# Kernel tuning notes

Hardware: AMD Instinct MI355X
Metric: run time of the kernel (lower is better)

## Reference

```python
import jax, jax.numpy as jnp
import numpy as np

NUM_EXPERTS = 8
M_TOTAL = 16384      # total routed tokens, sorted by expert
IN_FEATURES = 2048
OUT_FEATURES = 2048


def setup_inputs() -> dict:
    key = jax.random.key(0)
    k1, k2 = jax.random.split(key)
    x = jax.random.normal(k1, (M_TOTAL, IN_FEATURES), dtype=jnp.float32)
    # moe_fused_kaiming_uniform_: uniform(-sqrt(3*5/in), +sqrt(3*5/in))
    bound = float(np.sqrt(3.0 * 5.0 / IN_FEATURES))
    weight = jax.random.uniform(
        k2, (NUM_EXPERTS, OUT_FEATURES, IN_FEATURES),
        dtype=jnp.float32, minval=-bound, maxval=bound)
    # variable-size expert groups that sum exactly to M_TOTAL
    rng = np.random.default_rng(0)
    cuts = np.sort(rng.choice(np.arange(1, M_TOTAL), NUM_EXPERTS - 1, replace=False))
    m_sizes = np.diff(np.concatenate([[0], cuts, [M_TOTAL]])).astype(np.int32)
    return {"input": x, "weight": weight, "m_sizes": jnp.asarray(m_sizes)}


def reference(input, weight, m_sizes):
    """Grouped GEMM: rows of `input` are sorted by expert; the e-th contiguous
    block of m_sizes[e] rows is multiplied by weight[e].T ([out, in] -> x @ W_e^T)."""
    num_experts, out_features, _ = weight.shape
    m = input.shape[0]
    # per-token expert id from group sizes (jit-safe: fixed total length)
    expert_ids = jnp.repeat(jnp.arange(num_experts, dtype=jnp.int32), m_sizes,
                            total_repeat_length=m)  # [M]
    out = jnp.zeros((m, out_features), dtype=input.dtype)
    for e in range(num_experts):  # small fixed expert count
        mask = (expert_ids == e)[:, None]
        out = out + jnp.where(mask, input @ weight[e].T, jnp.zeros((), input.dtype))
    return out
```

## Files before the change

### kernel.cpp

```cpp
#include <hip/hip_runtime.h>
#include <hip/hip_bf16.h>

#define M_TOTAL 16384
#define KDIM 2048
#define NDIM 2048
#define NEXP 8
#define BM 256
#define BN 256
#define BK 32
#define MAX_ROW_TILES 71
#define NWG (MAX_ROW_TILES * 8)

typedef __attribute__((ext_vector_type(8))) __bf16 bf16x8;
typedef __attribute__((ext_vector_type(4))) float f32x4;

__device__ inline int minI(int a, int b) { return a < b ? a : b; }

__device__ inline bf16x8 cvt8(float4 a, float4 b) {
  bf16x8 r;
  r[0] = (__bf16)a.x; r[1] = (__bf16)a.y; r[2] = (__bf16)a.z; r[3] = (__bf16)a.w;
  r[4] = (__bf16)b.x; r[5] = (__bf16)b.y; r[6] = (__bf16)b.z; r[7] = (__bf16)b.w;
  return r;
}

__device__ inline void gload16(const void* g, void* l) {
  __builtin_amdgcn_global_load_lds(
      (const __attribute__((address_space(1))) void*)g,
      (__attribute__((address_space(3))) void*)l, 16, 0, 0);
}

__global__ __launch_bounds__(256) void cvt_both(
    const float* __restrict__ x, const float* __restrict__ w,
    bf16x8* __restrict__ xb, bf16x8* __restrict__ wb) {
  const int NX = (M_TOTAL * KDIM) / 8;
  const int NW = (NEXP * NDIM * KDIM) / 8;
  const int stride = gridDim.x * blockDim.x;
  for (int i = blockIdx.x * blockDim.x + threadIdx.x; i < NX + NW; i += stride) {
    const float4* src = (i < NX) ? ((const float4*)x + (size_t)i * 2)
                                 : ((const float4*)w + (size_t)(i - NX) * 2);
    float4 a = src[0], b = src[1];
    bf16x8 c = cvt8(a, b);
    if (i < NX) xb[i] = c; else wb[i - NX] = c;
  }
}

__global__ __launch_bounds__(512, 2) void moe_gemm_fr(
    const __hip_bfloat16* __restrict__ xb, const __hip_bfloat16* __restrict__ wb,
    const int* __restrict__ ms, float* __restrict__ out) {
  __shared__ __align__(16) char lds[131072];

  const int orig = blockIdx.x;
  const int wg = (orig & 7) * MAX_ROW_TILES + (orig >> 3);
  const int bt = wg >> 3;
  const int ntile = wg & 7;

  int sizes[NEXP];
#pragma unroll
  for (int i = 0; i < NEXP; ++i) sizes[i] = ms[i];
  int e = 0, row0 = 0, rows = 0, acc_t = 0, start = 0;
  bool found = false;
#pragma unroll
  for (int i = 0; i < NEXP; ++i) {
    int nt = (sizes[i] + BM - 1) >> 8;
    if (!found && bt < acc_t + nt) {
      found = true; e = i;
      int tt = bt - acc_t;
      row0 = start + tt * BM;
      rows = minI(sizes[i] - tt * BM, BM);
    }
    acc_t += nt; start += sizes[i];
  }
  if (!found) return;

  const int tid = threadIdx.x;
  const int lane = tid & 63;
  const int wave = tid >> 6;
  const int wr = wave >> 2, wc = wave & 3;
  const int col0 = ntile * BN;

  const int rwh = wave * 16 + (lane >> 2);
  const int colel = (((lane & 3) ^ ((lane >> 3) & 3)) << 3);
  const __hip_bfloat16* aS0 = xb + (size_t)minI(row0 + rwh, M_TOTAL - 1) * KDIM + colel;
  const __hip_bfloat16* aS1 = xb + (size_t)minI(row0 + 128 + rwh, M_TOTAL - 1) * KDIM + colel;
  const __hip_bfloat16* wbase = wb + (size_t)e * NDIM * KDIM;
  const __hip_bfloat16* bS0 = wbase + (size_t)(col0 + rwh) * KDIM + colel;
  const __hip_bfloat16* bS1 = wbase + (size_t)(col0 + 128 + rwh) * KDIM + colel;

  const int fr = lane & 15, fc = lane >> 4;
  const int laneOff = fr * 64 + ((fc ^ ((fr >> 1) & 3)) << 4);
  const int aOff = wr * 8192 + laneOff;
  const int bOff = 16384 + (wc >> 1) * 8192 + (wc & 1) * 4096 + laneOff;

  f32x4 acc[8][4];
  const f32x4 zero = {0.f, 0.f, 0.f, 0.f};
#pragma unroll
  for (int i = 0; i < 8; ++i)
#pragma unroll
    for (int j = 0; j < 4; ++j) acc[i][j] = zero;

#define ST4(BI, T) { char* b_ = lds + (BI) * 32768 + wave * 1024; \
    gload16(aS0 + (size_t)(T) * BK, b_); \
    gload16(aS1 + (size_t)(T) * BK, b_ + 8192); \
    gload16(bS0 + (size_t)(T) * BK, b_ + 16384); \
    gload16(bS1 + (size_t)(T) * BK, b_ + 24576); }
#define VM4 "vmcnt(4)"
#define VM0 "vmcnt(0)"

#define TILE(BI, T, DOST, VM) { \
    asm volatile("s_waitcnt " VM); \
    __builtin_amdgcn_s_barrier(); \
    if (DOST) ST4(((BI) + 2) & 3, (T) + 2); \
    const char* bb_ = lds + (BI) * 32768; \
    bf16x8 af[8], bv[4]; \
    bv[0] = *(const bf16x8*)(bb_ + bOff); \
    _Pragma("unroll") for (int mt = 0; mt < 8; ++mt) \
      af[mt] = *(const bf16x8*)(bb_ + aOff + mt * 1024); \
    _Pragma("unroll") for (int nt = 1; nt < 4; ++nt) \
      bv[nt] = *(const bf16x8*)(bb_ + bOff + nt * 1024); \
    __builtin_amdgcn_s_setprio(1); \
    _Pragma("unroll") for (int nt = 0; nt < 4; ++nt) \
      _Pragma("unroll") for (int mt = 0; mt < 8; ++mt) \
        acc[mt][nt] = __builtin_amdgcn_mfma_f32_16x16x32_bf16( \
            af[mt], bv[nt], acc[mt][nt], 0, 0, 0); \
    __builtin_amdgcn_s_setprio(0); \
  }

  ST4(0, 0)
  ST4(1, 1)

  for (int i = 0; i < 15; ++i) {
    const int t = 4 * i;
    TILE(0, t,     true, VM4)
    TILE(1, t + 1, true, VM4)
    TILE(2, t + 2, true, VM4)
    TILE(3, t + 3, true, VM4)
  }
  TILE(0, 60, true,  VM4)
  TILE(1, 61, true,  VM4)
  TILE(2, 62, false, VM4)
  TILE(3, 63, false, VM0)

#undef TILE
#undef VM0
#undef VM4
#undef ST4

  const int er = (lane >> 4) * 4;
#pragma unroll
  for (int mt = 0; mt < 8; ++mt) {
#pragma unroll
    for (int j = 0; j < 4; ++j) {
      int r = wr * 128 + mt * 16 + er + j;
      if (r < rows) {
        float* op = out + (size_t)(row0 + r) * NDIM + col0 + wc * 64 + (lane & 15);
#pragma unroll
        for (int nt = 0; nt < 4; ++nt) op[nt * 16] = acc[mt][nt][j];
      }
    }
  }
}

__global__ __launch_bounds__(256) void moe_gemm_f32(
    const float* __restrict__ x, const float* __restrict__ w,
    const int* __restrict__ ms, float* __restrict__ out) {
  __shared__ __align__(16) char As[128 * 64 * 2];
  __shared__ __align__(16) char Bs[128 * 64 * 2];
  int sizes[NEXP];
#pragma unroll
  for (int i = 0; i < NEXP; ++i) sizes[i] = ms[i];
  const int bt = blockIdx.y;
  int e = 0, row0 = 0, rows = 0, acc_t = 0, start = 0;
  bool found = false;
#pragma unroll
  for (int i = 0; i < NEXP; ++i) {
    int nt = (sizes[i] + 127) >> 7;
    if (!found && bt < acc_t + nt) {
      found = true; e = i;
      int tt = bt - acc_t;
      row0 = start + tt * 128;
      rows = minI(sizes[i] - tt * 128, 128);
    }
    acc_t += nt; start += sizes[i];
  }
  if (!found) return;
  const int tid = threadIdx.x;
  const int lane = tid & 63;
  const int wave = tid >> 6;
  const int wm = wave >> 1, wn = wave & 1;
  const int col0 = blockIdx.x * 128;
  const float* wbase = w + (size_t)e * (size_t)NDIM * KDIM;
  const int sr = tid >> 1;
  const int sh = tid & 1;
  const float* aptr = x + (size_t)(row0 + sr) * KDIM + sh * 32;
  const float* bptr = wbase + (size_t)(col0 + sr) * KDIM + sh * 32;
  const bool aval = (sr < rows);
  f32x4 acc[4][4];
  const f32x4 zero = {0.f, 0.f, 0.f, 0.f};
#pragma unroll
  for (int i = 0; i < 4; ++i)
#pragma unroll
    for (int j = 0; j < 4; ++j) acc[i][j] = zero;
  for (int kb = 0; kb < KDIM / 64; ++kb) {
    {
      float4 v[8];
      if (aval) {
        const float4* p = (const float4*)(aptr + kb * 64);
#pragma unroll
        for (int j = 0; j < 8; ++j) v[j] = p[j];
      } else {
#pragma unroll
        for (int j = 0; j < 8; ++j) v[j] = make_float4(0.f, 0.f, 0.f, 0.f);
      }
#pragma unroll
      for (int j = 0; j < 4; ++j) {
        bf16x8 c = cvt8(v[2 * j], v[2 * j + 1]);
        int chunk = (sh * 4 + j) ^ (sr & 7);
        *(bf16x8*)(As + sr * 128 + chunk * 16) = c;
      }
    }
    {
      const float4* p = (const float4*)(bptr + kb * 64);
      float4 u[8];
#pragma unroll
      for (int j = 0; j < 8; ++j) u[j] = p[j];
#pragma unroll
      for (int j = 0; j < 4; ++j) {
        bf16x8 c = cvt8(u[2 * j], u[2 * j + 1]);
        int chunk = (sh * 4 + j) ^ (sr & 7);
        *(bf16x8*)(Bs + sr * 128 + chunk * 16) = c;
      }
    }
    __syncthreads();
#pragma unroll
    for (int ks = 0; ks < 2; ++ks) {
      bf16x8 afr[4], bfv[4];
#pragma unroll
      for (int mt = 0; mt < 4; ++mt) {
        int r = wm * 64 + mt * 16 + (lane & 15);
        int chunk = (ks * 4 + (lane >> 4)) ^ (r & 7);
        afr[mt] = *(const bf16x8*)(As + r * 128 + chunk * 16);
      }
#pragma unroll
      for (int nt = 0; nt < 4; ++nt) {
        int r = wn * 64 + nt * 16 + (lane & 15);
        int chunk = (ks * 4 + (lane >> 4)) ^ (r & 7);
        bfv[nt] = *(const bf16x8*)(Bs + r * 128 + chunk * 16);
      }
#pragma unroll
      for (int mt = 0; mt < 4; ++mt)
#pragma unroll
        for (int nt = 0; nt < 4; ++nt)
          acc[mt][nt] = __builtin_amdgcn_mfma_f32_16x16x32_bf16(
              afr[mt], bfv[nt], acc[mt][nt], 0, 0, 0);
    }
    __syncthreads();
  }
#pragma unroll
  for (int mt = 0; mt < 4; ++mt) {
#pragma unroll
    for (int j = 0; j < 4; ++j) {
      int r = wm * 64 + mt * 16 + (lane >> 4) * 4 + j;
      if (r < rows) {
        float* op = out + (size_t)(row0 + r) * NDIM + col0 + wn * 64 + (lane & 15);
#pragma unroll
        for (int nt = 0; nt < 4; ++nt) op[nt * 16] = acc[mt][nt][j];
      }
    }
  }
}

extern "C" void kernel_launch(void* const* d_in, const int* in_sizes, int n_in,
                              void* d_out, int out_size, void* d_ws, size_t ws_size,
                              hipStream_t stream) {
  const float* x = (const float*)d_in[0];
  const float* w = (const float*)d_in[1];
  const int* ms = (const int*)d_in[2];
  float* out = (float*)d_out;
  const size_t nx = (size_t)M_TOTAL * KDIM;
  const size_t nw = (size_t)NEXP * NDIM * KDIM;
  const size_t need = (nx + nw) * sizeof(__hip_bfloat16);
  if (ws_size >= need) {
    __hip_bfloat16* xb = (__hip_bfloat16*)d_ws;
    __hip_bfloat16* wb = xb + nx;
    cvt_both<<<2048, 256, 0, stream>>>(x, w, (bf16x8*)xb, (bf16x8*)wb);
    moe_gemm_fr<<<dim3(NWG), dim3(512), 0, stream>>>(xb, wb, ms, out);
  } else {
    moe_gemm_f32<<<dim3(16, 135), dim3(256), 0, stream>>>(x, w, ms, out);
  }
}
```

Baseline: 249.0 us.

## Double-buffer A fragments in registers and deepen global prefetch to three tiles

The GEMM main loop now loads the A-operand fragments for the next K-tile from LDS into a second register set while the MFMAs for the current tile run, alternating between two register buffers. Global-to-LDS prefetch distance is raised from two tiles ahead to three, with a prologue that stages three tiles and preloads the first A fragments. The aim is to hide LDS read latency behind MFMA work and give global loads more slack. The cost is eight more bf16x8 registers per thread under a 2-waves-per-SIMD launch bound, which could cause spills, and tighter reuse of the four LDS buffers.

```diff
diff --git a/kernel.cpp b/kernel.cpp
--- a/kernel.cpp
+++ b/kernel.cpp
@@ -44,7 +44,7 @@
   }
 }
 
-__global__ __launch_bounds__(512, 2) void moe_gemm_fr(
+__global__ __launch_bounds__(512, 2) void moe_gemm_rdb(
     const __hip_bfloat16* __restrict__ xb, const __hip_bfloat16* __restrict__ wb,
     const int* __restrict__ ms, float* __restrict__ out) {
   __shared__ __align__(16) char lds[131072];
@@ -98,6 +98,8 @@
 #pragma unroll
     for (int j = 0; j < 4; ++j) acc[i][j] = zero;
 
+  bf16x8 afX[8], afY[8];
+
 #define ST4(BI, T) { char* b_ = lds + (BI) * 32768 + wave * 1024; \
     gload16(aS0 + (size_t)(T) * BK, b_); \
     gload16(aS1 + (size_t)(T) * BK, b_ + 8192); \
@@ -106,39 +108,45 @@
 #define VM4 "vmcnt(4)"
 #define VM0 "vmcnt(0)"
 
-#define TILE(BI, T, DOST, VM) { \
+#define TILE(T, VM, DOST, DOAF, CUR, NXT) { \
     asm volatile("s_waitcnt " VM); \
     __builtin_amdgcn_s_barrier(); \
-    if (DOST) ST4(((BI) + 2) & 3, (T) + 2); \
-    const char* bb_ = lds + (BI) * 32768; \
-    bf16x8 af[8], bv[4]; \
-    bv[0] = *(const bf16x8*)(bb_ + bOff); \
-    _Pragma("unroll") for (int mt = 0; mt < 8; ++mt) \
-      af[mt] = *(const bf16x8*)(bb_ + aOff + mt * 1024); \
-    _Pragma("unroll") for (int nt = 1; nt < 4; ++nt) \
-      bv[nt] = *(const bf16x8*)(bb_ + bOff + nt * 1024); \
+    if (DOST) ST4(((T) + 3) & 3, (T) + 3); \
+    const char* bcur_ = lds + ((T) & 3) * 32768; \
+    const char* bnxt_ = lds + (((T) + 1) & 3) * 32768; \
+    bf16x8 bv[4]; \
+    _Pragma("unroll") for (int nt = 0; nt < 4; ++nt) \
+      bv[nt] = *(const bf16x8*)(bcur_ + bOff + nt * 1024); \
+    if (DOAF) { _Pragma("unroll") for (int mt = 0; mt < 8; ++mt) \
+      af##NXT[mt] = *(const bf16x8*)(bnxt_ + aOff + mt * 1024); } \
     __builtin_amdgcn_s_setprio(1); \
     _Pragma("unroll") for (int nt = 0; nt < 4; ++nt) \
       _Pragma("unroll") for (int mt = 0; mt < 8; ++mt) \
         acc[mt][nt] = __builtin_amdgcn_mfma_f32_16x16x32_bf16( \
-            af[mt], bv[nt], acc[mt][nt], 0, 0, 0); \
+            af##CUR[mt], bv[nt], acc[mt][nt], 0, 0, 0); \
     __builtin_amdgcn_s_setprio(0); \
   }
 
   ST4(0, 0)
   ST4(1, 1)
+  ST4(2, 2)
+  asm volatile("s_waitcnt " VM4);
+  __builtin_amdgcn_s_barrier();
+#pragma unroll
+  for (int mt = 0; mt < 8; ++mt)
+    afX[mt] = *(const bf16x8*)(lds + aOff + mt * 1024);
 
   for (int i = 0; i < 15; ++i) {
     const int t = 4 * i;
-    TILE(0, t,     true, VM4)
-    TILE(1, t + 1, true, VM4)
-    TILE(2, t + 2, true, VM4)
-    TILE(3, t + 3, true, VM4)
-  }
-  TILE(0, 60, true,  VM4)
-  TILE(1, 61, true,  VM4)
-  TILE(2, 62, false, VM4)
-  TILE(3, 63, false, VM0)
+    TILE(t,     VM4, true, true, X, Y)
+    TILE(t + 1, VM4, true, true, Y, X)
+    TILE(t + 2, VM4, true, true, X, Y)
+    TILE(t + 3, VM4, true, true, Y, X)
+  }
+  TILE(60, VM4, true,  true,  X, Y)
+  TILE(61, VM4, false, true,  Y, X)
+  TILE(62, VM0, false, true,  X, Y)
+  TILE(63, VM0, false, false, Y, X)
 
 #undef TILE
 #undef VM0
@@ -283,7 +291,7 @@
     __hip_bfloat16* xb = (__hip_bfloat16*)d_ws;
     __hip_bfloat16* wb = xb + nx;
     cvt_both<<<2048, 256, 0, stream>>>(x, w, (bf16x8*)xb, (bf16x8*)wb);
-    moe_gemm_fr<<<dim3(NWG), dim3(512), 0, stream>>>(xb, wb, ms, out);
+    moe_gemm_rdb<<<dim3(NWG), dim3(512), 0, stream>>>(xb, wb, ms, out);
   } else {
     moe_gemm_f32<<<dim3(16, 135), dim3(256), 0, stream>>>(x, w, ms, out);
   }
```

Result: no change. 250.8 us (+0.7%).
